# Optimization experiments

Hardware: AMD Instinct MI355X
Metric: run time of the kernel (lower is better)

The kernel has to match this reference:

```python
import jax, jax.numpy as jnp
import numpy as np

# Fano plane lines (i, j, k): colonies whose octonion product should close, e_i * e_j ~ e_k
FANO = np.array([[0, 1, 3], [1, 2, 4], [2, 3, 5], [3, 4, 6], [4, 5, 0], [5, 6, 1], [6, 0, 2]], dtype=np.int64)


def _oct_structure():
    """8x8x8 structure constants M with (x*y)_k = sum_ij M[i,j,k] x_i y_j,
    built via Cayley-Dickson doubling of quaternions (true octonion multiply)."""
    def qmul(a, b):
        w1, x1, y1, z1 = a
        w2, x2, y2, z2 = b
        return np.array([
            w1 * w2 - x1 * x2 - y1 * y2 - z1 * z2,
            w1 * x2 + x1 * w2 + y1 * z2 - z1 * y2,
            w1 * y2 - x1 * z2 + y1 * w2 + z1 * x2,
            w1 * z2 + x1 * y2 - y1 * x2 + z1 * w2,
        ])

    def qconj(a):
        return a * np.array([1.0, -1.0, -1.0, -1.0])

    M = np.zeros((8, 8, 8), dtype=np.float32)
    I = np.eye(8, dtype=np.float32)
    for i in range(8):
        for j in range(8):
            a1, a2 = I[i, :4], I[i, 4:]
            b1, b2 = I[j, :4], I[j, 4:]
            c1 = qmul(a1, b1) - qmul(qconj(b2), a2)
            c2 = qmul(b2, a1) + qmul(a2, qconj(b1))
            M[i, j] = np.concatenate([c1, c2])
    return M


_M_NP = _oct_structure()


def setup_inputs() -> dict:
    key = jax.random.key(0)
    k1, = jax.random.split(key, 1)
    B = 1048576
    colony_states = jax.random.normal(k1, (B, 7, 8), dtype=jnp.float32)
    log_sensitivity = jnp.ones((), dtype=jnp.float32)  # nn.Parameter init 1.0
    return {"colony_states": colony_states, "log_sensitivity": log_sensitivity}


def reference(colony_states, log_sensitivity):
    M = jnp.asarray(_M_NP, dtype=colony_states.dtype)  # [8,8,8]
    # F.normalize(p=2, dim=-1): x / max(||x||, 1e-12)
    norm = jnp.maximum(jnp.linalg.norm(colony_states, axis=-1, keepdims=True), 1e-12)
    states = colony_states / norm  # [B,7,8]

    xi = states[:, FANO[:, 0]]  # [B,7,8]
    xj = states[:, FANO[:, 1]]  # [B,7,8]
    xk = states[:, FANO[:, 2]]  # [B,7,8]

    # All 7 Fano-line octonion products in one bilinear contraction
    prod = jnp.einsum('bli,blj,ijk->blk', xi, xj, M)  # [B,7,8]
    total_error = jnp.sum((prod - xk) ** 2, axis=(-1, -2))  # [B]
    avg_error = total_error / 7.0
    phi = -jnp.log(avg_error + 1e-8) * jnp.exp(log_sensitivity)
    return jnp.clip(phi, 0.0, 10.0)
```

## Files before the change

kernel.cpp:

```cpp
#include <hip/hip_runtime.h>
#include <math.h>
#include <stdint.h>

__device__ __forceinline__ void qmul(float w1, float x1, float y1, float z1,
                                     float w2, float x2, float y2, float z2,
                                     float& w, float& x, float& y, float& z) {
    w = w1 * w2 - x1 * x2 - y1 * y2 - z1 * z2;
    x = w1 * x2 + x1 * w2 + y1 * z2 - z1 * y2;
    y = w1 * y2 - x1 * z2 + y1 * w2 + z1 * x2;
    z = w1 * z2 + x1 * y2 - y1 * x2 + z1 * w2;
}

typedef __attribute__((address_space(3))) uint32_t lds_u32;
typedef const __attribute__((address_space(1))) uint32_t glb_u32;

__global__ __launch_bounds__(64) void oct_fano_kernel(
    const float* __restrict__ in,
    const float* __restrict__ logs,
    float* __restrict__ out,
    int B) {
    __shared__ __align__(16) float4 lds4[14 * 64];

    const int t = threadIdx.x;
    const int tile = blockIdx.x;
    const int nb = min(64, B - (tile << 6));

    const float4* gp = (const float4*)in;
    const long gbase = (long)tile * 896;
    const long gmax = (long)B * 14 - 1;
#pragma unroll
    for (int c = 0; c < 14; c++) {
        long idx = gbase + c * 64 + t;
        if (idx > gmax) idx = gmax;
        __builtin_amdgcn_global_load_lds((glb_u32*)(gp + idx),
                                         (lds_u32*)&lds4[c * 64], 16, 0, 0);
    }
    __builtin_amdgcn_s_waitcnt(0x0F70);
    __builtin_amdgcn_sched_barrier(0);

    if (t < nb) {
        float x[7][8];
#pragma unroll
        for (int k = 0; k < 14; k++) {
            float4 q = lds4[t * 14 + k];
            int r = k >> 1;
            int c = (k & 1) * 4;
            x[r][c + 0] = q.x;
            x[r][c + 1] = q.y;
            x[r][c + 2] = q.z;
            x[r][c + 3] = q.w;
        }

#pragma unroll
        for (int r = 0; r < 7; r++) {
            float s = 0.f;
#pragma unroll
            for (int c = 0; c < 8; c++) s += x[r][c] * x[r][c];
            float n = fmaxf(sqrtf(s), 1e-12f);
            float inv = 1.0f / n;
#pragma unroll
            for (int c = 0; c < 8; c++) x[r][c] *= inv;
        }

        float total = 0.f;
#pragma unroll
        for (int l = 0; l < 7; l++) {
            const float* a = x[l];
            const float* bb = x[(l + 1) % 7];
            const float* ck = x[(l + 3) % 7];

            float p0, p1, p2, p3, p4, p5, p6, p7;
            float t0, t1, t2, t3;
            qmul(a[0], a[1], a[2], a[3], bb[0], bb[1], bb[2], bb[3], p0, p1, p2, p3);
            qmul(bb[4], -bb[5], -bb[6], -bb[7], a[4], a[5], a[6], a[7], t0, t1, t2, t3);
            p0 -= t0; p1 -= t1; p2 -= t2; p3 -= t3;
            qmul(bb[4], bb[5], bb[6], bb[7], a[0], a[1], a[2], a[3], p4, p5, p6, p7);
            qmul(a[4], a[5], a[6], a[7], bb[0], -bb[1], -bb[2], -bb[3], t0, t1, t2, t3);
            p4 += t0; p5 += t1; p6 += t2; p7 += t3;

            float d0 = p0 - ck[0], d1 = p1 - ck[1], d2 = p2 - ck[2], d3 = p3 - ck[3];
            float d4 = p4 - ck[4], d5 = p5 - ck[5], d6 = p6 - ck[6], d7 = p7 - ck[7];
            total += d0 * d0 + d1 * d1 + d2 * d2 + d3 * d3 +
                     d4 * d4 + d5 * d5 + d6 * d6 + d7 * d7;
        }

        float avg = total * (1.0f / 7.0f);
        float phi = -logf(avg + 1e-8f) * expf(logs[0]);
        phi = fminf(fmaxf(phi, 0.0f), 10.0f);
        out[(tile << 6) + t] = phi;
    }
}

extern "C" void kernel_launch(void* const* d_in, const int* in_sizes, int n_in,
                              void* d_out, int out_size, void* d_ws, size_t ws_size,
                              hipStream_t stream) {
    const float* states = (const float*)d_in[0];
    const float* logs = (const float*)d_in[1];
    float* out = (float*)d_out;
    int B = in_sizes[0] / 56;
    int ntiles = (B + 63) / 64;
    oct_fano_kernel<<<ntiles, 64, 0, stream>>>(states, logs, out, B);
}
```

Measured before the change: 313.4 us.

## Use persistent blocks with double-buffered async LDS prefetch and padded layout

Replaces the one-tile-per-block grid with 1280 persistent 64-thread blocks that loop over tiles, prefetching the next tile into a second LDS buffer with global_load_lds while the current one is computed. The LDS pages are padded to 65 float4 to cut bank conflicts on the strided per-thread reads. It also swaps in rsqrt, fast log/exp and hoists the sensitivity exponent out of the loop. The goal is to hide global-load latency in this memory-bound kernel, at the cost of fewer resident waves and a partial-waitcnt scheme that relies on in-order vmcnt accounting.

Result: slower. 322.1 us (+2.8%).

```diff
diff --git a/kernel.cpp b/kernel.cpp
--- a/kernel.cpp
+++ b/kernel.cpp
@@ -14,80 +14,111 @@
 typedef __attribute__((address_space(3))) uint32_t lds_u32;
 typedef const __attribute__((address_space(1))) uint32_t glb_u32;
 
+#define PAGE 65
+#define BUFG (14 * PAGE)
+
 __global__ __launch_bounds__(64) void oct_fano_kernel(
     const float* __restrict__ in,
     const float* __restrict__ logs,
     float* __restrict__ out,
-    int B) {
-    __shared__ __align__(16) float4 lds4[14 * 64];
+    int B, int ntiles) {
+    __shared__ __align__(16) float4 lds4[2 * BUFG];
 
     const int t = threadIdx.x;
-    const int tile = blockIdx.x;
-    const int nb = min(64, B - (tile << 6));
+    const int G = gridDim.x;
+    const float4* gp = (const float4*)in;
+    const long gmax = (long)B * 14 - 1;
+    const float sens = __expf(logs[0]);
 
-    const float4* gp = (const float4*)in;
-    const long gbase = (long)tile * 896;
-    const long gmax = (long)B * 14 - 1;
+    int tile = blockIdx.x;
+    int p = 0;
+
+    if (tile < ntiles) {
+        const long gbase = (long)tile * 896;
 #pragma unroll
-    for (int c = 0; c < 14; c++) {
-        long idx = gbase + c * 64 + t;
-        if (idx > gmax) idx = gmax;
-        __builtin_amdgcn_global_load_lds((glb_u32*)(gp + idx),
-                                         (lds_u32*)&lds4[c * 64], 16, 0, 0);
+        for (int c = 0; c < 14; c++) {
+            long idx = gbase + c * 64 + t;
+            if (idx > gmax) idx = gmax;
+            __builtin_amdgcn_global_load_lds((glb_u32*)(gp + idx),
+                                             (lds_u32*)&lds4[c * PAGE], 16, 0, 0);
+        }
     }
-    __builtin_amdgcn_s_waitcnt(0x0F70);
-    __builtin_amdgcn_sched_barrier(0);
 
-    if (t < nb) {
-        float x[7][8];
+    while (tile < ntiles) {
+        const int next = tile + G;
+        const float4* __restrict__ cur = &lds4[p * BUFG];
+
+        if (next < ntiles) {
+            float4* nxt = &lds4[(p ^ 1) * BUFG];
+            const long gbase = (long)next * 896;
 #pragma unroll
-        for (int k = 0; k < 14; k++) {
-            float4 q = lds4[t * 14 + k];
-            int r = k >> 1;
-            int c = (k & 1) * 4;
-            x[r][c + 0] = q.x;
-            x[r][c + 1] = q.y;
-            x[r][c + 2] = q.z;
-            x[r][c + 3] = q.w;
+            for (int c = 0; c < 14; c++) {
+                long idx = gbase + c * 64 + t;
+                if (idx > gmax) idx = gmax;
+                __builtin_amdgcn_global_load_lds((glb_u32*)(gp + idx),
+                                                 (lds_u32*)&nxt[c * PAGE], 16, 0, 0);
+            }
+            __builtin_amdgcn_s_waitcnt(0x0F7E);
+        } else {
+            __builtin_amdgcn_s_waitcnt(0x0F70);
+        }
+        __builtin_amdgcn_sched_barrier(0);
+
+        const int nb = min(64, B - (tile << 6));
+        if (t < nb) {
+            float x[7][8];
+#pragma unroll
+            for (int k = 0; k < 14; k++) {
+                int g = t * 14 + k;
+                float4 q = cur[g + (g >> 6)];
+                int r = k >> 1;
+                int c = (k & 1) * 4;
+                x[r][c + 0] = q.x;
+                x[r][c + 1] = q.y;
+                x[r][c + 2] = q.z;
+                x[r][c + 3] = q.w;
+            }
+
+#pragma unroll
+            for (int r = 0; r < 7; r++) {
+                float s = 0.f;
+#pragma unroll
+                for (int c = 0; c < 8; c++) s += x[r][c] * x[r][c];
+                float inv = rsqrtf(fmaxf(s, 1e-24f));
+#pragma unroll
+                for (int c = 0; c < 8; c++) x[r][c] *= inv;
+            }
+
+            float total = 0.f;
+#pragma unroll
+            for (int l = 0; l < 7; l++) {
+                const float* a = x[l];
+                const float* bb = x[(l + 1) % 7];
+                const float* ck = x[(l + 3) % 7];
+
+                float p0, p1, p2, p3, p4, p5, p6, p7;
+                float t0, t1, t2, t3;
+                qmul(a[0], a[1], a[2], a[3], bb[0], bb[1], bb[2], bb[3], p0, p1, p2, p3);
+                qmul(bb[4], -bb[5], -bb[6], -bb[7], a[4], a[5], a[6], a[7], t0, t1, t2, t3);
+                p0 -= t0; p1 -= t1; p2 -= t2; p3 -= t3;
+                qmul(bb[4], bb[5], bb[6], bb[7], a[0], a[1], a[2], a[3], p4, p5, p6, p7);
+                qmul(a[4], a[5], a[6], a[7], bb[0], -bb[1], -bb[2], -bb[3], t0, t1, t2, t3);
+                p4 += t0; p5 += t1; p6 += t2; p7 += t3;
+
+                float d0 = p0 - ck[0], d1 = p1 - ck[1], d2 = p2 - ck[2], d3 = p3 - ck[3];
+                float d4 = p4 - ck[4], d5 = p5 - ck[5], d6 = p6 - ck[6], d7 = p7 - ck[7];
+                total += d0 * d0 + d1 * d1 + d2 * d2 + d3 * d3 +
+                         d4 * d4 + d5 * d5 + d6 * d6 + d7 * d7;
+            }
+
+            float avg = total * (1.0f / 7.0f);
+            float phi = -__logf(avg + 1e-8f) * sens;
+            phi = fminf(fmaxf(phi, 0.0f), 10.0f);
+            out[(tile << 6) + t] = phi;
         }
 
-#pragma unroll
-        for (int r = 0; r < 7; r++) {
-            float s = 0.f;
-#pragma unroll
-            for (int c = 0; c < 8; c++) s += x[r][c] * x[r][c];
-            float n = fmaxf(sqrtf(s), 1e-12f);
-            float inv = 1.0f / n;
-#pragma unroll
-            for (int c = 0; c < 8; c++) x[r][c] *= inv;
-        }
-
-        float total = 0.f;
-#pragma unroll
-        for (int l = 0; l < 7; l++) {
-            const float* a = x[l];
-            const float* bb = x[(l + 1) % 7];
-            const float* ck = x[(l + 3) % 7];
-
-            float p0, p1, p2, p3, p4, p5, p6, p7;
-            float t0, t1, t2, t3;
-            qmul(a[0], a[1], a[2], a[3], bb[0], bb[1], bb[2], bb[3], p0, p1, p2, p3);
-            qmul(bb[4], -bb[5], -bb[6], -bb[7], a[4], a[5], a[6], a[7], t0, t1, t2, t3);
-            p0 -= t0; p1 -= t1; p2 -= t2; p3 -= t3;
-            qmul(bb[4], bb[5], bb[6], bb[7], a[0], a[1], a[2], a[3], p4, p5, p6, p7);
-            qmul(a[4], a[5], a[6], a[7], bb[0], -bb[1], -bb[2], -bb[3], t0, t1, t2, t3);
-            p4 += t0; p5 += t1; p6 += t2; p7 += t3;
-
-            float d0 = p0 - ck[0], d1 = p1 - ck[1], d2 = p2 - ck[2], d3 = p3 - ck[3];
-            float d4 = p4 - ck[4], d5 = p5 - ck[5], d6 = p6 - ck[6], d7 = p7 - ck[7];
-            total += d0 * d0 + d1 * d1 + d2 * d2 + d3 * d3 +
-                     d4 * d4 + d5 * d5 + d6 * d6 + d7 * d7;
-        }
-
-        float avg = total * (1.0f / 7.0f);
-        float phi = -logf(avg + 1e-8f) * expf(logs[0]);
-        phi = fminf(fmaxf(phi, 0.0f), 10.0f);
-        out[(tile << 6) + t] = phi;
+        p ^= 1;
+        tile = next;
     }
 }
 
@@ -99,5 +130,7 @@
     float* out = (float*)d_out;
     int B = in_sizes[0] / 56;
     int ntiles = (B + 63) / 64;
-    oct_fano_kernel<<<ntiles, 64, 0, stream>>>(states, logs, out, B);
+    int nblocks = 256 * 5;
+    if (nblocks > ntiles) nblocks = ntiles;
+    oct_fano_kernel<<<nblocks, 64, 0, stream>>>(states, logs, out, B, ntiles);
 }
```
